# Performance work log

Measured on AMD Instinct MI355X. Metric: run time of the kernel, lower is better.

The kernel has to match this reference:

```python
import jax, jax.numpy as jnp
import numpy as np

ENT_TOTAL = 100000
REL_TOTAL = 1000
ENT_SIZE = 200
REL_SIZE = 200
BATCH = 16384
MARGIN = 4.0


def setup_inputs() -> dict:
    key = jax.random.key(0)
    ks = jax.random.split(key, 8)
    return {
        "pos_h": jax.random.randint(ks[0], (BATCH,), 0, ENT_TOTAL, dtype=jnp.int32),
        "pos_t": jax.random.randint(ks[1], (BATCH,), 0, ENT_TOTAL, dtype=jnp.int32),
        "pos_r": jax.random.randint(ks[2], (BATCH,), 0, REL_TOTAL, dtype=jnp.int32),
        "neg_h": jax.random.randint(ks[3], (BATCH,), 0, ENT_TOTAL, dtype=jnp.int32),
        "neg_t": jax.random.randint(ks[4], (BATCH,), 0, ENT_TOTAL, dtype=jnp.int32),
        "ent_emb": jax.random.normal(ks[5], (ENT_TOTAL, ENT_SIZE), dtype=jnp.float32) * 0.1,
        "rel_emb": jax.random.normal(ks[6], (REL_TOTAL, REL_SIZE), dtype=jnp.float32) * 0.1,
        "transfer": jax.random.normal(ks[7], (REL_TOTAL, ENT_SIZE * REL_SIZE), dtype=jnp.float32) * 0.05,
    }


def _l2norm(x):
    # tf.nn.l2_normalize semantics: x / sqrt(max(sum(x^2), eps))
    return x * jax.lax.rsqrt(jnp.maximum(jnp.sum(x * x, axis=-1, keepdims=True), 1e-12))


def _calc(h, t, r):
    return jnp.abs(_l2norm(h) + _l2norm(r) - _l2norm(t))


def reference(pos_h, pos_t, pos_r, neg_h, neg_t, ent_emb, rel_emb, transfer):
    # gather embeddings
    pos_h_e = ent_emb[pos_h]                 # [b, ent]
    pos_t_e = ent_emb[pos_t]
    pos_r_e = rel_emb[pos_r]                 # [b, rel]
    neg_h_e = ent_emb[neg_h]
    neg_t_e = ent_emb[neg_t]
    # relation-specific transfer matrices [b, ent, rel]
    pos_mat = transfer[pos_r].reshape(-1, ENT_SIZE, REL_SIZE)
    # project entities into relation space: [b, ent] x [b, ent, rel] -> [b, rel]
    p_h = jnp.einsum('be,ber->br', pos_h_e, pos_mat)
    p_t = jnp.einsum('be,ber->br', pos_t_e, pos_mat)
    n_h = jnp.einsum('be,ber->br', neg_h_e, pos_mat)  # negative_rel == 0: reuse pos matrix
    n_t = jnp.einsum('be,ber->br', neg_t_e, pos_mat)
    p_score = jnp.sum(_calc(p_h, p_t, pos_r_e), axis=-1, keepdims=True)  # [b,1]
    n_score = jnp.sum(_calc(n_h, n_t, pos_r_e), axis=-1, keepdims=True)
    loss = jnp.mean(jnp.maximum(p_score - n_score + MARGIN, 0.0))
    return loss
```

## Files before the change

kernel.cpp:

```cpp
#include <hip/hip_runtime.h>

#define ENT 200
#define RELD 200
#define NREL 1000
#define NBATCH 16384
#define MARGIN 4.0f
#define CHUNK 32
#define NVEC 128
#define MAXCHUNKS 1512

#define BSTRIDE_I 211
#define BBUF 844

#define WS_NCHUNKS 3072
#define WS_CHUNKS 3076
#define WS_LIST 11268
#define WS_ELEM 27652

typedef __attribute__((ext_vector_type(8))) short short8;
typedef __attribute__((ext_vector_type(4))) float floatx4;

__device__ __forceinline__ unsigned short f2bf(float x) {
    unsigned u = __float_as_uint(x);
    u = (u + 0x7FFFu + ((u >> 16) & 1u)) >> 16;
    return (unsigned short)u;
}

__device__ __forceinline__ float wave_reduce(float v) {
#pragma unroll
    for (int off = 32; off > 0; off >>= 1) v += __shfl_down(v, off, 64);
    return v;
}

__global__ __launch_bounds__(1024) void prep_kernel(const int* __restrict__ pos_r,
                                                    int* __restrict__ ws) {
    __shared__ int cnt_s[NREL];
    __shared__ int off_s[NREL];
    __shared__ int scan_s[1024];
    const int tid = threadIdx.x;

    for (int i = tid; i < NREL; i += 1024) cnt_s[i] = 0;
    __syncthreads();

    int rl[16];
#pragma unroll
    for (int k = 0; k < 16; ++k) {
        rl[k] = pos_r[(k << 10) + tid];
        atomicAdd(&cnt_s[rl[k]], 1);
    }
    __syncthreads();

    const int cnt = (tid < NREL) ? cnt_s[tid] : 0;

    scan_s[tid] = cnt;
    __syncthreads();
#pragma unroll
    for (int off = 1; off < 1024; off <<= 1) {
        const int add = (tid >= off) ? scan_s[tid - off] : 0;
        __syncthreads();
        scan_s[tid] += add;
        __syncthreads();
    }
    const int myoff = scan_s[tid] - cnt;
    if (tid < NREL) off_s[tid] = myoff;
    __syncthreads();

    const int nch = (cnt + CHUNK - 1) / CHUNK;
    scan_s[tid] = nch;
    __syncthreads();
#pragma unroll
    for (int off = 1; off < 1024; off <<= 1) {
        const int add = (tid >= off) ? scan_s[tid - off] : 0;
        __syncthreads();
        scan_s[tid] += add;
        __syncthreads();
    }
    const int cbase = scan_s[tid] - nch;
    int4* chunks = (int4*)(ws + WS_CHUNKS);
    for (int k = 0; k < nch; ++k)
        chunks[cbase + k] = make_int4(tid, myoff + CHUNK * k, min(CHUNK, cnt - CHUNK * k), 0);
    if (tid == 1023) ws[WS_NCHUNKS] = scan_s[1023];

    if (tid < NREL) cnt_s[tid] = 0;
    __syncthreads();
#pragma unroll
    for (int k = 0; k < 16; ++k) {
        const int r = rl[k];
        const int p = off_s[r] + atomicAdd(&cnt_s[r], 1);
        ws[WS_LIST + p] = (k << 10) + tid;
    }
}

__global__ __launch_bounds__(512) void transr_mfma_kernel(
    const int* __restrict__ pos_h, const int* __restrict__ pos_t,
    const int* __restrict__ neg_h, const int* __restrict__ neg_t,
    const float* __restrict__ ent_emb, const float* __restrict__ rel_emb,
    const float* __restrict__ transfer, int* __restrict__ ws)
{
    const int nch = ws[WS_NCHUNKS];
    const int stride = (nch + 7) >> 3;
    const int bidx = blockIdx.x;
    if ((bidx >> 3) >= stride) return;
    const int cix = (bidx & 7) * stride + (bidx >> 3);
    if (cix >= nch) return;

    __shared__ short sB[2 * BBUF * 8];
    __shared__ int items_s[CHUNK];
    __shared__ int rows[NVEC];

    const int4 ck = ((const int4*)(ws + WS_CHUNKS))[cix];
    const int r = ck.x, start = ck.y, cnt = ck.z;

    const int tid  = threadIdx.x;
    const int lane = tid & 63;
    const int wv   = tid >> 6;
    const int q    = lane >> 4;
    const int n    = lane & 15;
    const bool wactive = (wv * 4 < cnt);

    if (tid < CHUNK) items_s[tid] = ws[WS_LIST + start + min(tid, cnt - 1)];
    __syncthreads();
    if (tid < NVEC) {
        const int b = items_s[tid >> 2];
        const int c = tid & 3;
        rows[tid] = (c == 0) ? pos_h[b] : (c == 1) ? pos_t[b] : (c == 2) ? neg_h[b] : neg_t[b];
    }
    __syncthreads();

    short8 afrag[7];
#pragma unroll
    for (int s = 0; s < 7; ++s) afrag[s] = (short8){0, 0, 0, 0, 0, 0, 0, 0};
    if (wactive) {
        const int row = rows[wv * 16 + n];
        const float* __restrict__ ab = ent_emb + (size_t)row * ENT;
#pragma unroll
        for (int s = 0; s < 7; ++s) {
            const int e0 = s * 32 + q * 8;
            if (e0 < ENT) {
                float v[8];
                *(float4*)(&v[0]) = *(const float4*)(ab + e0);
                *(float4*)(&v[4]) = *(const float4*)(ab + e0 + 4);
                short8 f;
#pragma unroll
                for (int j = 0; j < 8; ++j) f[j] = (short)f2bf(v[j]);
                afrag[s] = f;
            }
        }
    }

    const int slot = tid;
    const int sq   = slot / 52;
    const int srem = slot - sq * 52;
    const int scol = srem * 4;
    const bool sact = (slot < 208) && (scol < RELD);
    const float* __restrict__ Mb = transfer + (size_t)r * (ENT * RELD) + scol;
    const int k0 = sq * 8;

    float fm[8][4];
    short8 bh[4];
#define LOAD_SLAB(s_)                                                          \
    {                                                                          \
        const int kk = (s_) * 32 + k0;                                         \
        if (sact && kk < ENT) {                                                \
            _Pragma("unroll")                                                  \
            for (int j = 0; j < 8; ++j)                                        \
                *(float4*)(&fm[j][0]) = *(const float4*)(Mb + (size_t)(kk + j) * RELD); \
        } else {                                                               \
            _Pragma("unroll")                                                  \
            for (int j = 0; j < 8; ++j) {                                      \
                fm[j][0] = 0.f; fm[j][1] = 0.f; fm[j][2] = 0.f; fm[j][3] = 0.f;\
            }                                                                  \
        }                                                                      \
    }
#define CONV_SLAB()                                                            \
    {                                                                          \
        _Pragma("unroll")                                                      \
        for (int i = 0; i < 4; ++i) {                                          \
            short8 f;                                                          \
            _Pragma("unroll")                                                  \
            for (int j = 0; j < 8; ++j) f[j] = (short)f2bf(fm[j][i]);          \
            bh[i] = f;                                                         \
        }                                                                      \
    }
#define WRITE_SLAB(buf_)                                                       \
    if (slot < 208) {                                                          \
        _Pragma("unroll")                                                      \
        for (int i = 0; i < 4; ++i)                                            \
            *(short8*)(&sB[((buf_) * BBUF + i * BSTRIDE_I + slot) * 8]) = bh[i]; \
    }

    floatx4 acc[13];
#pragma unroll
    for (int c = 0; c < 13; ++c) acc[c] = (floatx4){0.f, 0.f, 0.f, 0.f};

    const int rb16 = (n & 3) * BSTRIDE_I + q * 52 + (n >> 2);

    LOAD_SLAB(0); CONV_SLAB(); WRITE_SLAB(0);
    LOAD_SLAB(1); CONV_SLAB();
    __syncthreads();

#pragma unroll
    for (int s = 0; s < 7; ++s) {
        if (s < 5) LOAD_SLAB(s + 2);
        if (wactive) {
            const int bb = (s & 1) * BBUF;
#pragma unroll
            for (int c = 0; c < 13; ++c) {
                const short8 bf = *(const short8*)(&sB[(bb + rb16 + c * 4) * 8]);
                acc[c] = __builtin_amdgcn_mfma_f32_16x16x32_bf16(afrag[s], bf, acc[c], 0, 0, 0);
            }
        }
        if (s < 6) WRITE_SLAB((s + 1) & 1);
        if (s < 5) CONV_SLAB();
        if (s < 6) __syncthreads();
    }

    if (wactive) {
        float rl[13];
        const float* __restrict__ rb = rel_emb + (size_t)r * RELD;
#pragma unroll
        for (int c = 0; c < 13; ++c) {
            const int col = c * 16 + n;
            rl[c] = (col < RELD) ? rb[col] : 0.f;
        }
        float nsq[4] = {0.f, 0.f, 0.f, 0.f};
        float rsq = 0.f;
#pragma unroll
        for (int c = 0; c < 13; ++c) {
            nsq[0] += acc[c][0] * acc[c][0];
            nsq[1] += acc[c][1] * acc[c][1];
            nsq[2] += acc[c][2] * acc[c][2];
            nsq[3] += acc[c][3] * acc[c][3];
            rsq += rl[c] * rl[c];
        }
#pragma unroll
        for (int m = 1; m < 16; m <<= 1) {
#pragma unroll
            for (int k = 0; k < 4; ++k) nsq[k] += __shfl_xor(nsq[k], m, 64);
            rsq += __shfl_xor(rsq, m, 64);
        }
        float inv[4];
#pragma unroll
        for (int k = 0; k < 4; ++k) inv[k] = rsqrtf(fmaxf(nsq[k], 1e-12f));
        const float invr = rsqrtf(fmaxf(rsq, 1e-12f));

        float psum = 0.f, nsum = 0.f;
#pragma unroll
        for (int c = 0; c < 13; ++c) {
            const float rr = rl[c] * invr;
            psum += fabsf(acc[c][0] * inv[0] + rr - acc[c][1] * inv[1]);
            nsum += fabsf(acc[c][2] * inv[2] + rr - acc[c][3] * inv[3]);
        }
#pragma unroll
        for (int m = 1; m < 16; m <<= 1) {
            psum += __shfl_xor(psum, m, 64);
            nsum += __shfl_xor(nsum, m, 64);
        }
        const int item = wv * 4 + q;
        if (n == 0 && item < cnt) {
            float* elem = (float*)(ws + WS_ELEM);
            elem[items_s[item]] = fmaxf(psum - nsum + MARGIN, 0.f);
        }
    }
}

__global__ __launch_bounds__(256) void reduce_mean_kernel(const int* __restrict__ ws,
                                                          float* __restrict__ out) {
    __shared__ float sred[4];
    const float4* elem = (const float4*)(ws + WS_ELEM);
    float s = 0.f;
    for (int i = threadIdx.x; i < NBATCH / 4; i += 256) {
        const float4 v = elem[i];
        s += v.x + v.y + v.z + v.w;
    }
    s = wave_reduce(s);
    const int lane = threadIdx.x & 63;
    const int wvv = threadIdx.x >> 6;
    if (lane == 0) sred[wvv] = s;
    __syncthreads();
    if (threadIdx.x == 0)
        out[0] = (sred[0] + sred[1] + sred[2] + sred[3]) * (1.0f / (float)NBATCH);
}

extern "C" void kernel_launch(void* const* d_in, const int* in_sizes, int n_in,
                              void* d_out, int out_size, void* d_ws, size_t ws_size,
                              hipStream_t stream) {
    const int* pos_h = (const int*)d_in[0];
    const int* pos_t = (const int*)d_in[1];
    const int* pos_r = (const int*)d_in[2];
    const int* neg_h = (const int*)d_in[3];
    const int* neg_t = (const int*)d_in[4];
    const float* ent_emb = (const float*)d_in[5];
    const float* rel_emb = (const float*)d_in[6];
    const float* transfer = (const float*)d_in[7];

    int* ws = (int*)d_ws;
    float* out = (float*)d_out;

    prep_kernel<<<1, 1024, 0, stream>>>(pos_r, ws);
    transr_mfma_kernel<<<MAXCHUNKS, 512, 0, stream>>>(
        pos_h, pos_t, neg_h, neg_t, ent_emb, rel_emb, transfer, ws);
    reduce_mean_kernel<<<1, 256, 0, stream>>>(ws, out);
}
```

Baseline: 319.3 us.

## Stage 64-row slabs of the transfer matrix per pipeline step

```diff
diff --git a/kernel.cpp b/kernel.cpp
--- a/kernel.cpp
+++ b/kernel.cpp
@@ -9,8 +9,9 @@
 #define NVEC 128
 #define MAXCHUNKS 1512
 
-#define BSTRIDE_I 211
-#define BBUF 844
+#define NSLOT 416
+#define BSTRIDE_I 419
+#define BBUF 1676
 
 #define WS_NCHUNKS 3072
 #define WS_CHUNKS 3076
@@ -152,15 +153,15 @@
     const int sq   = slot / 52;
     const int srem = slot - sq * 52;
     const int scol = srem * 4;
-    const bool sact = (slot < 208) && (scol < RELD);
+    const bool sact = (slot < NSLOT) && (scol < RELD);
     const float* __restrict__ Mb = transfer + (size_t)r * (ENT * RELD) + scol;
     const int k0 = sq * 8;
 
     float fm[8][4];
     short8 bh[4];
-#define LOAD_SLAB(s_)                                                          \
+#define LOAD_SLAB(p_)                                                          \
     {                                                                          \
-        const int kk = (s_) * 32 + k0;                                         \
+        const int kk = (p_) * 64 + k0;                                         \
         if (sact && kk < ENT) {                                                \
             _Pragma("unroll")                                                  \
             for (int j = 0; j < 8; ++j)                                        \
@@ -183,7 +184,7 @@
         }                                                                      \
     }
 #define WRITE_SLAB(buf_)                                                       \
-    if (slot < 208) {                                                          \
+    if (slot < NSLOT) {                                                        \
         _Pragma("unroll")                                                      \
         for (int i = 0; i < 4; ++i)                                            \
             *(short8*)(&sB[((buf_) * BBUF + i * BSTRIDE_I + slot) * 8]) = bh[i]; \
@@ -200,19 +201,24 @@
     __syncthreads();
 
 #pragma unroll
-    for (int s = 0; s < 7; ++s) {
-        if (s < 5) LOAD_SLAB(s + 2);
+    for (int p = 0; p < 4; ++p) {
+        if (p < 2) LOAD_SLAB(p + 2);
         if (wactive) {
-            const int bb = (s & 1) * BBUF;
-#pragma unroll
-            for (int c = 0; c < 13; ++c) {
-                const short8 bf = *(const short8*)(&sB[(bb + rb16 + c * 4) * 8]);
-                acc[c] = __builtin_amdgcn_mfma_f32_16x16x32_bf16(afrag[s], bf, acc[c], 0, 0, 0);
+            const int bb = (p & 1) * BBUF;
+#pragma unroll
+            for (int ks = 0; ks < 2; ++ks) {
+                if (p * 64 + ks * 32 < ENT) {
+#pragma unroll
+                    for (int c = 0; c < 13; ++c) {
+                        const short8 bf = *(const short8*)(&sB[(bb + rb16 + ks * 208 + c * 4) * 8]);
+                        acc[c] = __builtin_amdgcn_mfma_f32_16x16x32_bf16(afrag[2 * p + ks], bf, acc[c], 0, 0, 0);
+                    }
+                }
             }
         }
-        if (s < 6) WRITE_SLAB((s + 1) & 1);
-        if (s < 5) CONV_SLAB();
-        if (s < 6) __syncthreads();
+        if (p < 3) WRITE_SLAB((p + 1) & 1);
+        if (p < 2) CONV_SLAB();
+        if (p < 3) __syncthreads();
     }
 
     if (wactive) {
```

After: 319.2 us. About the same (-0.0%).
